# Kernel tuning notes

Measured on AMD Instinct MI355X. Metric: run time of the kernel, lower is better.

## Reference

```python
import jax, jax.numpy as jnp
import numpy as np

B_, N, C, H, WS, NW = 2048, 49, 384, 12, 7, 64
D = C // H  # head_dim = 32
SCALE = D ** -0.5


def _relative_position_index(ws=WS):
    coords = np.stack(np.meshgrid(np.arange(ws), np.arange(ws), indexing='ij'))  # [2,ws,ws]
    flat = coords.reshape(2, -1)                         # [2, N]
    rel = flat[:, :, None] - flat[:, None, :]            # [2, N, N]
    rel = rel.transpose(1, 2, 0)                         # [N, N, 2]
    rel[..., 0] += ws - 1
    rel[..., 1] += ws - 1
    rel[..., 0] *= 2 * ws - 1
    return rel.sum(-1).astype(np.int32)                  # [N, N]


def setup_inputs() -> dict:
    key = jax.random.key(0)
    ks = jax.random.split(key, 9)
    return {
        'x1': jax.random.normal(ks[0], (B_, N, C), jnp.float32),
        'x2': jax.random.normal(ks[1], (B_, N, C), jnp.float32),
        'mask1': jax.random.normal(ks[2], (NW, N, N), jnp.float32),
        'mask2': jax.random.normal(ks[3], (NW, N, N), jnp.float32),
        'w_qkv': jax.random.normal(ks[4], (C, 3 * C), jnp.float32) * 0.02,
        'b_qkv': jax.random.normal(ks[5], (3 * C,), jnp.float32) * 0.02,
        'w_proj': jax.random.normal(ks[6], (C, C), jnp.float32) * 0.02,
        'b_proj': jax.random.normal(ks[7], (C,), jnp.float32) * 0.02,
        'rpb_table': jax.random.normal(ks[8], ((2 * WS - 1) ** 2, H), jnp.float32) * 0.02,
        'rel_index': jnp.asarray(_relative_position_index()),
    }


def _qkv(x, w_qkv, b_qkv):
    # x: [B_, N, C] -> q,k,v each [B_, H, N, D]
    qkv = (x @ w_qkv + b_qkv).reshape(B_, N, 3, H, D).transpose(2, 0, 3, 1, 4)
    return qkv[0], qkv[1], qkv[2]


def reference(x1, x2, mask1, mask2, w_qkv, b_qkv, w_proj, b_proj, rpb_table, rel_index):
    # relative position bias: [H, N, N]
    rpb = rpb_table[rel_index.reshape(-1)].reshape(N, N, H).transpose(2, 0, 1)

    q1, k1, v1 = _qkv(x1, w_qkv, b_qkv)
    _, k2, v2 = _qkv(x2, w_qkv, b_qkv)
    q1s = q1 * SCALE

    attn1 = jnp.einsum('bhnd,bhmd->bhnm', q1s, k1) + rpb[None]
    attn2 = jnp.einsum('bhnd,bhmd->bhnm', q1s, k2) + rpb[None]  # note: q1, per source

    # shifted-window mask add: [B_//nW, nW, H, N, N] + mask[None, :, None]
    attn1 = (attn1.reshape(B_ // NW, NW, H, N, N) + mask1[None, :, None]).reshape(B_, H, N, N)
    attn2 = (attn2.reshape(B_ // NW, NW, H, N, N) + mask2[None, :, None]).reshape(B_, H, N, N)

    attn = jax.nn.softmax(jnp.concatenate([attn1, attn2], axis=1), axis=-1)  # [B_, 2H, N, N]

    v = jnp.concatenate([v1, v2], axis=1)  # [B_, 2H, N, D]
    out = jnp.einsum('bhnm,bhmd->bhnd', attn, v)
    weights = out.transpose(0, 2, 1, 3).reshape(B_, N, 2 * C)
    x = weights[:, :, :C] @ w_proj + b_proj
    return x, weights
```

## Files before the change

kernel.cpp:

```cpp
#include <hip/hip_runtime.h>

typedef unsigned short u16;
typedef unsigned int u32;
typedef __attribute__((ext_vector_type(8))) short short8;
typedef __attribute__((ext_vector_type(4))) float f32x4;

#define NB 2048
#define NTOK 49
#define CH 384
#define NH 12
#define HD 32
#define SCALE_Q 0.17677669529663687f
#define TABF 1956864

__device__ __forceinline__ u16 f2bf(float f) {
  u32 u = __float_as_uint(f);
  u += 0x7fffu + ((u >> 16) & 1u);
  return (u16)(u >> 16);
}
__device__ __forceinline__ float bf2f(u16 h) { return __uint_as_float(((u32)h) << 16); }
__device__ __forceinline__ u32 pk2(float a, float b) { return (u32)f2bf(a) | ((u32)f2bf(b) << 16); }

__device__ __forceinline__ void gload16(const u16* g, u16* l) {
  __builtin_amdgcn_global_load_lds(
      (const __attribute__((address_space(1))) u32*)g,
      (__attribute__((address_space(3))) u32*)l,
      16, 0, 0);
}

__global__ void prep_w(const float* __restrict__ w_qkv, const float* __restrict__ w_proj,
                       u16* __restrict__ wqkvT, u16* __restrict__ wprojT)
{
  int idx = blockIdx.x * 256 + threadIdx.x;
  if (idx < 1152 * 384) {
    int n = idx / 384, k = idx - n * 384;
    wqkvT[idx] = f2bf(w_qkv[(size_t)k * 1152 + n]);
  } else if (idx < 1152 * 384 + 384 * 384) {
    int i2 = idx - 1152 * 384;
    int n = i2 / 384, k = i2 - n * 384;
    wprojT[i2] = f2bf(w_proj[(size_t)k * 384 + n]);
  }
}

__global__ __launch_bounds__(256) void prep_c(const float* __restrict__ rpb_table,
                                              const int* __restrict__ rel_index,
                                              const float* __restrict__ mask1,
                                              const float* __restrict__ mask2,
                                              float* __restrict__ comb)
{
  const int wbh = blockIdx.x;
  const int wb = wbh / 12, h = wbh - wb * 12;
  const size_t ob = (size_t)wbh * (49 * 52);
  for (int r = threadIdx.x; r < 2401; r += 256) {
    int i = r / 49, j = r - i * 49;
    float rv = rpb_table[(size_t)rel_index[r] * 12 + h];
    comb[ob + i * 52 + j]        = rv + mask1[(size_t)wb * 2401 + r];
    comb[TABF + ob + i * 52 + j] = rv + mask2[(size_t)wb * 2401 + r];
  }
}

__global__ __launch_bounds__(256) void conv_bf16(const float* __restrict__ x1, const float* __restrict__ x2,
                                                 u16* __restrict__ xb1, u16* __restrict__ xb2)
{
  const size_t i = ((size_t)blockIdx.x * 256 + threadIdx.x) * 8;
  float4 a = *reinterpret_cast<const float4*>(x1 + i);
  float4 b = *reinterpret_cast<const float4*>(x1 + i + 4);
  uint4 o;
  o.x = pk2(a.x, a.y); o.y = pk2(a.z, a.w); o.z = pk2(b.x, b.y); o.w = pk2(b.z, b.w);
  *reinterpret_cast<uint4*>(xb1 + i) = o;
  a = *reinterpret_cast<const float4*>(x2 + i);
  b = *reinterpret_cast<const float4*>(x2 + i + 4);
  o.x = pk2(a.x, a.y); o.y = pk2(a.z, a.w); o.z = pk2(b.x, b.y); o.w = pk2(b.z, b.w);
  *reinterpret_cast<uint4*>(xb2 + i) = o;
}

__global__ __launch_bounds__(512) void gemm_qkv(
    const u16* __restrict__ xb1, const u16* __restrict__ xb2,
    const u16* __restrict__ wT, const float* __restrict__ bias,
    u16* __restrict__ q1, u16* __restrict__ k1, u16* __restrict__ v1,
    u16* __restrict__ k2, u16* __restrict__ v2)
{
  __shared__ __align__(16) u16 smem[38912];
  u16* Cs = smem;

  const int bid0 = blockIdx.x;
  const int lin = (bid0 & 7) * 735 + (bid0 >> 3);
  const int mt = lin / 15;
  const int nt = lin - mt * 15;

  const bool isx2 = nt >= 9;
  const u16* __restrict__ X = isx2 ? xb2 : xb1;
  const int colbase = isx2 ? 384 + (nt - 9) * 128 : nt * 128;
  const int m0 = mt * 256;
  const int tid = threadIdx.x;
  const int lane = tid & 63, w = tid >> 6;
  const int wm = w & 3, wn = w >> 2;
  const int l15 = lane & 15, l4 = lane >> 4;

  f32x4 acc[4][4] = {};

  const u16* ga = X + (size_t)(m0 + l15) * CH + l4 * 8;
  const u16* gb = wT + (size_t)(colbase + w * 16 + l15) * CH + l4 * 8;
  const int ga0 = (2 * w) * 16 * CH, ga1 = (2 * w + 1) * 16 * CH;

  auto stage = [&](int bs, int kk) {
    u16* A = smem + bs * 12288;
    u16* B = A + 8192;
    gload16(ga + kk + ga0, &A[(2 * w) * 512]);
    gload16(ga + kk + ga1, &A[(2 * w + 1) * 512]);
    gload16(gb + kk, &B[w * 512]);
  };

  stage(0, 0);
  stage(1, 32);
  stage(2, 64);

#pragma unroll
  for (int k = 0; k < 12; ++k) {
    if (k <= 9)       asm volatile("s_waitcnt vmcnt(6)" ::: "memory");
    else if (k == 10) asm volatile("s_waitcnt vmcnt(3)" ::: "memory");
    else              asm volatile("s_waitcnt vmcnt(0)" ::: "memory");
    __builtin_amdgcn_s_barrier();
    __builtin_amdgcn_sched_barrier(0);
    const int cb = k % 3;
    const u16* A = smem + cb * 12288;
    const u16* B = A + 8192;
    short8 af[4], bfr[4];
#pragma unroll
    for (int i = 0; i < 4; ++i)
      af[i] = *reinterpret_cast<const short8*>(&A[(wm * 4 + i) * 512 + lane * 8]);
#pragma unroll
    for (int j = 0; j < 4; ++j)
      bfr[j] = *reinterpret_cast<const short8*>(&B[(wn * 4 + j) * 512 + lane * 8]);
#pragma unroll
    for (int i = 0; i < 4; ++i)
#pragma unroll
      for (int j = 0; j < 4; ++j)
        acc[i][j] = __builtin_amdgcn_mfma_f32_16x16x32_bf16(af[i], bfr[j], acc[i][j], 0, 0, 0);
    asm volatile("s_waitcnt lgkmcnt(0)" ::: "memory");
    __builtin_amdgcn_s_barrier();
    __builtin_amdgcn_sched_barrier(0);
    if (k + 3 < 12) stage(cb, (k + 3) * 32);
  }

#pragma unroll
  for (int j = 0; j < 4; ++j) {
    const int colL = wn * 64 + j * 16 + l15;
    const int gcol = colbase + colL;
    const float bb = bias[gcol];
    const float scl = (gcol < 384) ? SCALE_Q : 1.0f;
#pragma unroll
    for (int i = 0; i < 4; ++i)
#pragma unroll
      for (int r = 0; r < 4; ++r) {
        const int row = wm * 64 + i * 16 + l4 * 4 + r;
        Cs[row * 152 + (colL ^ (((row >> 2) & 3) << 3))] = f2bf((acc[i][j][r] + bb) * scl);
      }
  }
  __syncthreads();

  u16* dst;
  int tb;
  if (colbase < 384)      { dst = q1;              tb = colbase; }
  else if (colbase < 768) { dst = isx2 ? k2 : k1;  tb = colbase - 384; }
  else                    { dst = isx2 ? v2 : v1;  tb = colbase - 768; }

#pragma unroll
  for (int u = 0; u < 8; ++u) {
    const int pc = tid + u * 512;
    const int row = pc >> 4, pp = pc & 15;
    const uint4 val = *reinterpret_cast<const uint4*>(&Cs[row * 152 + ((pp ^ ((row >> 2) & 3)) << 3)]);
    const int gm = m0 + row;
    const int b = gm / 49, tok = gm - b * 49;
    const int cm = tb + pp * 8;
    const int h = cm >> 5, d0 = cm & 31;
    *reinterpret_cast<uint4*>(&dst[(((size_t)b * NH + h) * NTOK + tok) * HD + d0]) = val;
  }
}

__global__ __launch_bounds__(256) void attn_kernel(
    const u16* __restrict__ q1, const u16* __restrict__ k1, const u16* __restrict__ v1,
    const u16* __restrict__ k2, const u16* __restrict__ v2,
    const float* __restrict__ comb, float* __restrict__ outw)
{
  __shared__ __align__(16) u16 VT[2][32][72];
  __shared__ __align__(16) u16 Pb[4][2][512];

  const int h = blockIdx.x, b = blockIdx.y;
  const int tid = threadIdx.x;
  const int lane = tid & 63, wt = tid >> 6;
  const int l15 = lane & 15, l4 = lane >> 4;
  const size_t base = ((size_t)b * NH + h) * 1568;

  for (int e = tid; e < 392; e += 256) {
    const int p = e >= 196;
    const int e2 = e - p * 196;
    const int tok = e2 >> 2, d8 = (e2 & 3) * 8;
    const u16* src = (p ? v2 : v1) + base + tok * 32 + d8;
    uint4 val = *reinterpret_cast<const uint4*>(src);
    const u16* pv = reinterpret_cast<const u16*>(&val);
#pragma unroll
    for (int q = 0; q < 8; ++q) VT[p][d8 + q][tok] = pv[q];
  }
  for (int e = tid; e < 2 * 32 * 15; e += 256) {
    int p = (e >= 480) ? 1 : 0;
    int e2 = e - p * 480;
    int d = e2 / 15, j = 49 + (e2 - d * 15);
    VT[p][d][j] = 0;
  }

  const short8 aq = *reinterpret_cast<const short8*>(&q1[base + (wt * 16 + l15) * 32 + l4 * 8]);

  __syncthreads();

  const int wb = b & 63;
  const int irow = wt * 16 + l15;
  const float* cb0 = comb + ((size_t)(wb * 12 + h) * 49 + (irow < 49 ? irow : 48)) * 52;
  const size_t obase = (size_t)b * (NTOK * 768) + (size_t)h * 32;

#pragma unroll
  for (int p = 0; p < 2; ++p) {
    const u16* __restrict__ kp = p ? k2 : k1;
    const float* cbp = cb0 + (size_t)p * TABF;

    f32x4 st[4];
    __builtin_amdgcn_s_setprio(1);
#pragma unroll
    for (int jt = 0; jt < 4; ++jt) {
      short8 bk = *reinterpret_cast<const short8*>(&kp[base + (jt * 16 + l15) * 32 + l4 * 8]);
      st[jt] = __builtin_amdgcn_mfma_f32_16x16x32_bf16(bk, aq, (f32x4){0.f, 0.f, 0.f, 0.f}, 0, 0, 0);
    }
    __builtin_amdgcn_s_setprio(0);

#pragma unroll
    for (int jt = 0; jt < 4; ++jt) {
      const float4 c = *reinterpret_cast<const float4*>(cbp + jt * 16 + l4 * 4);
#pragma unroll
      for (int r = 0; r < 4; ++r) {
        const int j = jt * 16 + l4 * 4 + r;
        st[jt][r] = (j < 49) ? st[jt][r] + (&c.x)[r] : -1e30f;
      }
    }

    float mx = -1e30f;
#pragma unroll
    for (int jt = 0; jt < 4; ++jt)
#pragma unroll
      for (int r = 0; r < 4; ++r) mx = fmaxf(mx, st[jt][r]);
    mx = fmaxf(mx, __shfl_xor(mx, 16));
    mx = fmaxf(mx, __shfl_xor(mx, 32));
    float sm = 0.f;
#pragma unroll
    for (int jt = 0; jt < 4; ++jt)
#pragma unroll
      for (int r = 0; r < 4; ++r) {
        float e = __expf(st[jt][r] - mx);
        st[jt][r] = e;
        sm += e;
      }
    sm += __shfl_xor(sm, 16);
    sm += __shfl_xor(sm, 32);
    const float si = 1.f / sm;

#pragma unroll
    for (int jt = 0; jt < 4; ++jt) {
      const int kt = jt >> 1;
#pragma unroll
      for (int r = 0; r < 4; r += 2) {
        const u32 pkv = pk2(st[jt][r] * si, st[jt][r + 1] * si);
        const int jrel = (jt & 1) * 16 + l4 * 4 + r;
        const int off = ((jrel >> 3) << 7) + l15 * 8 + (jrel & 7);
        *reinterpret_cast<u32*>(&Pb[wt][kt][off]) = pkv;
      }
    }

    f32x4 o[2] = {};
    __builtin_amdgcn_s_setprio(1);
#pragma unroll
    for (int kt = 0; kt < 2; ++kt) {
      short8 ap = *reinterpret_cast<const short8*>(&Pb[wt][kt][lane * 8]);
#pragma unroll
      for (int n2 = 0; n2 < 2; ++n2) {
        short8 bvf = *reinterpret_cast<const short8*>(&VT[p][n2 * 16 + l15][kt * 32 + l4 * 8]);
        o[n2] = __builtin_amdgcn_mfma_f32_16x16x32_bf16(bvf, ap, o[n2], 0, 0, 0);
      }
    }
    __builtin_amdgcn_s_setprio(0);

    const int i = wt * 16 + l15;
    if (i < 49) {
#pragma unroll
      for (int n2 = 0; n2 < 2; ++n2) {
        float4 vst = {o[n2][0], o[n2][1], o[n2][2], o[n2][3]};
        *reinterpret_cast<float4*>(&outw[obase + (size_t)i * 768 + p * 384 + n2 * 16 + l4 * 4]) = vst;
      }
    }
  }
}

__global__ __launch_bounds__(256) void gemm_proj(
    const float* __restrict__ Wsrc, const u16* __restrict__ wT,
    const float* __restrict__ bias, float* __restrict__ outx)
{
  __shared__ __align__(16) u16 smem[24576];
  const int bid0 = blockIdx.x;
  const int lin = (bid0 & 7) * 294 + (bid0 >> 3);
  const int mt = lin / 3;
  const int nt = lin - mt * 3;

  const int colbase = nt * 128;
  const int m0 = mt * 128;
  const int tid = threadIdx.x;
  const int lane = tid & 63, wv = tid >> 6;
  const int wr = wv >> 1, wc = wv & 1;
  const int l15 = lane & 15, l4 = lane >> 4;

  f32x4 acc[4][4] = {};

  const float* ga = Wsrc + (size_t)(m0 + l15) * 768 + l4 * 8;
  const u16*   gb = wT + (size_t)(colbase + l15) * CH + l4 * 8;
  const int g0 = wv, g1 = wv + 4;

  float4 ar0[2][2], ar1[2][2], ar2[2][2];
  auto loadA = [&](float4 (*ar)[2], int kk) {
    ar[0][0] = *reinterpret_cast<const float4*>(ga + kk + g0 * 16 * 768);
    ar[0][1] = *reinterpret_cast<const float4*>(ga + kk + g0 * 16 * 768 + 4);
    ar[1][0] = *reinterpret_cast<const float4*>(ga + kk + g1 * 16 * 768);
    ar[1][1] = *reinterpret_cast<const float4*>(ga + kk + g1 * 16 * 768 + 4);
  };
  auto stageB = [&](int bs, int kk) {
    u16* B = smem + bs * 8192 + 4096;
    gload16(gb + kk + g0 * 16 * CH, B + g0 * 512);
    gload16(gb + kk + g1 * 16 * CH, B + g1 * 512);
  };
  auto writeA = [&](float4 (*ar)[2], int bs) {
    u16* A = smem + bs * 8192;
    uint4 v;
    v.x = pk2(ar[0][0].x, ar[0][0].y); v.y = pk2(ar[0][0].z, ar[0][0].w);
    v.z = pk2(ar[0][1].x, ar[0][1].y); v.w = pk2(ar[0][1].z, ar[0][1].w);
    *reinterpret_cast<uint4*>(&A[g0 * 512 + lane * 8]) = v;
    v.x = pk2(ar[1][0].x, ar[1][0].y); v.y = pk2(ar[1][0].z, ar[1][0].w);
    v.z = pk2(ar[1][1].x, ar[1][1].y); v.w = pk2(ar[1][1].z, ar[1][1].w);
    *reinterpret_cast<uint4*>(&A[g1 * 512 + lane * 8]) = v;
  };

  loadA(ar0, 0);  stageB(0, 0);
  loadA(ar1, 32); stageB(1, 32);
  loadA(ar2, 64); stageB(2, 64);

#pragma unroll
  for (int k = 0; k < 12; ++k) {
    if (k <= 9)       asm volatile("s_waitcnt vmcnt(12)" ::: "memory");
    else if (k == 10) asm volatile("s_waitcnt vmcnt(6)" ::: "memory");
    else              asm volatile("s_waitcnt vmcnt(0)" ::: "memory");
    const int cb = k % 3;
    if (cb == 0) writeA(ar0, 0);
    else if (cb == 1) writeA(ar1, 1);
    else writeA(ar2, 2);
    asm volatile("s_waitcnt lgkmcnt(0)" ::: "memory");
    __builtin_amdgcn_s_barrier();
    __builtin_amdgcn_sched_barrier(0);
    const u16* A = smem + cb * 8192;
    const u16* B = A + 4096;
    short8 af[4], bfr[4];
#pragma unroll
    for (int i = 0; i < 4; ++i)
      af[i] = *reinterpret_cast<const short8*>(&A[(wr * 4 + i) * 512 + lane * 8]);
#pragma unroll
    for (int j = 0; j < 4; ++j)
      bfr[j] = *reinterpret_cast<const short8*>(&B[(wc * 4 + j) * 512 + lane * 8]);
#pragma unroll
    for (int i = 0; i < 4; ++i)
#pragma unroll
      for (int j = 0; j < 4; ++j)
        acc[i][j] = __builtin_amdgcn_mfma_f32_16x16x32_bf16(af[i], bfr[j], acc[i][j], 0, 0, 0);
    asm volatile("s_waitcnt lgkmcnt(0)" ::: "memory");
    __builtin_amdgcn_s_barrier();
    __builtin_amdgcn_sched_barrier(0);
    if (k + 3 < 12) {
      if (cb == 0)      loadA(ar0, (k + 3) * 32);
      else if (cb == 1) loadA(ar1, (k + 3) * 32);
      else              loadA(ar2, (k + 3) * 32);
      stageB(cb, (k + 3) * 32);
    }
  }

#pragma unroll
  for (int j = 0; j < 4; ++j) {
    const int col = colbase + wc * 64 + j * 16 + l15;
    const float bb = bias[col];
#pragma unroll
    for (int i = 0; i < 4; ++i) {
#pragma unroll
      for (int r = 0; r < 4; ++r) {
        const int gm = m0 + wr * 64 + i * 16 + l4 * 4 + r;
        outx[(size_t)gm * CH + col] = acc[i][j][r] + bb;
      }
    }
  }
}

extern "C" void kernel_launch(void* const* d_in, const int* in_sizes, int n_in,
                              void* d_out, int out_size, void* d_ws, size_t ws_size,
                              hipStream_t stream) {
  const float* x1        = (const float*)d_in[0];
  const float* x2        = (const float*)d_in[1];
  const float* mask1     = (const float*)d_in[2];
  const float* mask2     = (const float*)d_in[3];
  const float* w_qkv     = (const float*)d_in[4];
  const float* b_qkv     = (const float*)d_in[5];
  const float* w_proj    = (const float*)d_in[6];
  const float* b_proj    = (const float*)d_in[7];
  const float* rpb_table = (const float*)d_in[8];
  const int*   rel_index = (const int*)d_in[9];

  float* outx = (float*)d_out;
  const size_t SZe = (size_t)NB * NH * NTOK * HD;
  float* outw = outx + SZe;

  u16* q1 = (u16*)d_out;
  u16* k1 = q1 + SZe;
  u16* xb1 = (u16*)outw;
  u16* xb2 = xb1 + SZe;

  u16* v1 = (u16*)d_ws;
  u16* k2 = v1 + SZe;
  u16* v2 = k2 + SZe;
  u16* wqkvT  = v2 + SZe;
  u16* wprojT = wqkvT + 1152 * 384;
  float* comb = (float*)(wprojT + 384 * 384);

  prep_w<<<2304, 256, 0, stream>>>(w_qkv, w_proj, wqkvT, wprojT);
  prep_c<<<768, 256, 0, stream>>>(rpb_table, rel_index, mask1, mask2, comb);
  conv_bf16<<<(int)(SZe / (256 * 8)), 256, 0, stream>>>(x1, x2, xb1, xb2);
  gemm_qkv<<<5880, 512, 0, stream>>>(xb1, xb2, wqkvT, b_qkv, q1, k1, v1, k2, v2);
  attn_kernel<<<dim3(12, 2048), 256, 0, stream>>>(q1, k1, v1, k2, v2, comb, outw);
  gemm_proj<<<2352, 256, 0, stream>>>(outw, wprojT, b_proj, outx);
}
```

Measured before the change: 723.0 us.

## Fuse fp32-to-bf16 conversion of activations into QKV GEMM A-tile loading

Removes the standalone conversion kernel and instead loads fp32 activations directly in the QKV GEMM, converting to bf16 in registers before writing A tiles to shared memory. This eliminates a full pass that wrote and reread a bf16 copy of both inputs. In exchange, each GEMM block reads twice as many A bytes from fp32, uses more registers for the three in-flight A buffers, and replaces async direct-to-LDS loads with register-staged stores.

```diff
diff --git a/kernel.cpp b/kernel.cpp
--- a/kernel.cpp
+++ b/kernel.cpp
@@ -59,23 +59,8 @@
   }
 }
 
-__global__ __launch_bounds__(256) void conv_bf16(const float* __restrict__ x1, const float* __restrict__ x2,
-                                                 u16* __restrict__ xb1, u16* __restrict__ xb2)
-{
-  const size_t i = ((size_t)blockIdx.x * 256 + threadIdx.x) * 8;
-  float4 a = *reinterpret_cast<const float4*>(x1 + i);
-  float4 b = *reinterpret_cast<const float4*>(x1 + i + 4);
-  uint4 o;
-  o.x = pk2(a.x, a.y); o.y = pk2(a.z, a.w); o.z = pk2(b.x, b.y); o.w = pk2(b.z, b.w);
-  *reinterpret_cast<uint4*>(xb1 + i) = o;
-  a = *reinterpret_cast<const float4*>(x2 + i);
-  b = *reinterpret_cast<const float4*>(x2 + i + 4);
-  o.x = pk2(a.x, a.y); o.y = pk2(a.z, a.w); o.z = pk2(b.x, b.y); o.w = pk2(b.z, b.w);
-  *reinterpret_cast<uint4*>(xb2 + i) = o;
-}
-
 __global__ __launch_bounds__(512) void gemm_qkv(
-    const u16* __restrict__ xb1, const u16* __restrict__ xb2,
+    const float* __restrict__ x1, const float* __restrict__ x2,
     const u16* __restrict__ wT, const float* __restrict__ bias,
     u16* __restrict__ q1, u16* __restrict__ k1, u16* __restrict__ v1,
     u16* __restrict__ k2, u16* __restrict__ v2)
@@ -89,7 +74,7 @@
   const int nt = lin - mt * 15;
 
   const bool isx2 = nt >= 9;
-  const u16* __restrict__ X = isx2 ? xb2 : xb1;
+  const float* __restrict__ X = isx2 ? x2 : x1;
   const int colbase = isx2 ? 384 + (nt - 9) * 128 : nt * 128;
   const int m0 = mt * 256;
   const int tid = threadIdx.x;
@@ -99,30 +84,48 @@
 
   f32x4 acc[4][4] = {};
 
-  const u16* ga = X + (size_t)(m0 + l15) * CH + l4 * 8;
-  const u16* gb = wT + (size_t)(colbase + w * 16 + l15) * CH + l4 * 8;
+  const float* ga = X + (size_t)(m0 + l15) * CH + l4 * 8;
+  const u16*   gb = wT + (size_t)(colbase + w * 16 + l15) * CH + l4 * 8;
   const int ga0 = (2 * w) * 16 * CH, ga1 = (2 * w + 1) * 16 * CH;
 
-  auto stage = [&](int bs, int kk) {
+  float4 ar0[2][2], ar1[2][2], ar2[2][2];
+  auto loadA = [&](float4 (*ar)[2], int kk) {
+    ar[0][0] = *reinterpret_cast<const float4*>(ga + ga0 + kk);
+    ar[0][1] = *reinterpret_cast<const float4*>(ga + ga0 + kk + 4);
+    ar[1][0] = *reinterpret_cast<const float4*>(ga + ga1 + kk);
+    ar[1][1] = *reinterpret_cast<const float4*>(ga + ga1 + kk + 4);
+  };
+  auto stageB = [&](int bs, int kk) {
+    u16* B = smem + bs * 12288 + 8192;
+    gload16(gb + kk, &B[w * 512]);
+  };
+  auto writeA = [&](float4 (*ar)[2], int bs) {
     u16* A = smem + bs * 12288;
-    u16* B = A + 8192;
-    gload16(ga + kk + ga0, &A[(2 * w) * 512]);
-    gload16(ga + kk + ga1, &A[(2 * w + 1) * 512]);
-    gload16(gb + kk, &B[w * 512]);
-  };
-
-  stage(0, 0);
-  stage(1, 32);
-  stage(2, 64);
+    uint4 v;
+    v.x = pk2(ar[0][0].x, ar[0][0].y); v.y = pk2(ar[0][0].z, ar[0][0].w);
+    v.z = pk2(ar[0][1].x, ar[0][1].y); v.w = pk2(ar[0][1].z, ar[0][1].w);
+    *reinterpret_cast<uint4*>(&A[(2 * w) * 512 + lane * 8]) = v;
+    v.x = pk2(ar[1][0].x, ar[1][0].y); v.y = pk2(ar[1][0].z, ar[1][0].w);
+    v.z = pk2(ar[1][1].x, ar[1][1].y); v.w = pk2(ar[1][1].z, ar[1][1].w);
+    *reinterpret_cast<uint4*>(&A[(2 * w + 1) * 512 + lane * 8]) = v;
+  };
+
+  loadA(ar0, 0);  stageB(0, 0);
+  loadA(ar1, 32); stageB(1, 32);
+  loadA(ar2, 64); stageB(2, 64);
 
 #pragma unroll
   for (int k = 0; k < 12; ++k) {
-    if (k <= 9)       asm volatile("s_waitcnt vmcnt(6)" ::: "memory");
-    else if (k == 10) asm volatile("s_waitcnt vmcnt(3)" ::: "memory");
+    if (k <= 9)       asm volatile("s_waitcnt vmcnt(10)" ::: "memory");
+    else if (k == 10) asm volatile("s_waitcnt vmcnt(5)" ::: "memory");
     else              asm volatile("s_waitcnt vmcnt(0)" ::: "memory");
+    const int cb = k % 3;
+    if (cb == 0)      writeA(ar0, 0);
+    else if (cb == 1) writeA(ar1, 1);
+    else              writeA(ar2, 2);
+    asm volatile("s_waitcnt lgkmcnt(0)" ::: "memory");
     __builtin_amdgcn_s_barrier();
     __builtin_amdgcn_sched_barrier(0);
-    const int cb = k % 3;
     const u16* A = smem + cb * 12288;
     const u16* B = A + 8192;
     short8 af[4], bfr[4];
@@ -140,7 +143,12 @@
     asm volatile("s_waitcnt lgkmcnt(0)" ::: "memory");
     __builtin_amdgcn_s_barrier();
     __builtin_amdgcn_sched_barrier(0);
-    if (k + 3 < 12) stage(cb, (k + 3) * 32);
+    if (k + 3 < 12) {
+      if (cb == 0)      loadA(ar0, (k + 3) * 32);
+      else if (cb == 1) loadA(ar1, (k + 3) * 32);
+      else              loadA(ar2, (k + 3) * 32);
+      stageB(cb, (k + 3) * 32);
+    }
   }
 
 #pragma unroll
@@ -420,8 +428,6 @@
 
   u16* q1 = (u16*)d_out;
   u16* k1 = q1 + SZe;
-  u16* xb1 = (u16*)outw;
-  u16* xb2 = xb1 + SZe;
 
   u16* v1 = (u16*)d_ws;
   u16* k2 = v1 + SZe;
@@ -432,8 +438,7 @@
 
   prep_w<<<2304, 256, 0, stream>>>(w_qkv, w_proj, wqkvT, wprojT);
   prep_c<<<768, 256, 0, stream>>>(rpb_table, rel_index, mask1, mask2, comb);
-  conv_bf16<<<(int)(SZe / (256 * 8)), 256, 0, stream>>>(x1, x2, xb1, xb2);
-  gemm_qkv<<<5880, 512, 0, stream>>>(xb1, xb2, wqkvT, b_qkv, q1, k1, v1, k2, v2);
+  gemm_qkv<<<5880, 512, 0, stream>>>(x1, x2, wqkvT, b_qkv, q1, k1, v1, k2, v2);
   attn_kernel<<<dim3(12, 2048), 256, 0, stream>>>(q1, k1, v1, k2, v2, comb, outw);
   gemm_proj<<<2352, 256, 0, stream>>>(outw, wprojT, b_proj, outx);
 }
```

Result: slower. 910.7 us (+26.0%).
